# Optimization experiments

Hardware: AMD Instinct MI355X
Metric: run time of the kernel (lower is better)

The kernel has to match this reference:

```python
import jax, jax.numpy as jnp
import numpy as np

# Hough voting constants from the call site:
# Hough(angle=90, R2_list=[4,64,256,1024], num_classes=1, region_num=13, vote_field_size=33)
ANGLE = 90
R2_LIST = (4, 64, 256, 1024)
REGION_NUM = 13
VFS = 33  # vote field size


def _hough_filter():
    """Log-polar vote-field filter [region_num, VFS, VFS].

    Region 0 = center disk (r^2 <= R2_LIST[0]); region 1 + ring*4 + angle_bin
    for the 3 radius rings x 4 angle sectors. Each region's weights are
    1/(#pixels in region) so each region's vote sums to 1 (HoughNet log map).
    """
    c = VFS // 2
    ys, xs = np.meshgrid(np.arange(VFS) - c, np.arange(VFS) - c, indexing='ij')
    r2 = xs ** 2 + ys ** 2
    theta = (np.degrees(np.arctan2(ys, xs)) + 360.0) % 360.0
    nang = 360 // ANGLE  # 4 angle sectors
    abin = np.minimum((theta // ANGLE).astype(np.int64), nang - 1)
    region = -np.ones((VFS, VFS), np.int64)
    region[r2 <= R2_LIST[0]] = 0
    for i in range(1, len(R2_LIST)):
        m = (r2 > R2_LIST[i - 1]) & (r2 <= R2_LIST[i])
        region[m] = 1 + (i - 1) * nang + abin[m]
    filt = np.zeros((REGION_NUM, VFS, VFS), np.float32)
    for r in range(REGION_NUM):
        m = region == r
        if m.sum() > 0:
            filt[r][m] = 1.0 / float(m.sum())
    return filt


# ConvTranspose2d(13 -> 1, k=33, stride=1, pad=16) == SAME conv with flipped kernel.
_HOUGH_CONV_W = jnp.asarray(np.flip(_hough_filter(), axis=(1, 2))[None].copy())  # [1,13,33,33]


def setup_inputs() -> dict:
    key = jax.random.key(0)
    ks = jax.random.split(key, 4)
    B, C, H, W = 2, 256, 256, 512
    return {
        'x': jax.random.normal(ks[0], (B, C, H, W), jnp.float32),
        'pos_w': jax.random.normal(ks[1], (13, C), jnp.float32) * 0.05,
        'pos_b': jnp.zeros((13,), jnp.float32),
        'reg_w': jax.random.normal(ks[2], (1, C), jnp.float32) * 0.05,
        'reg_b': jnp.zeros((1,), jnp.float32),
        'off_w': jax.random.normal(ks[3], (2, C), jnp.float32) * 0.05,
        'off_b': jnp.zeros((2,), jnp.float32),
    }


def _conv1x1(x, w, b):
    # x: [B,C,H,W], w: [O,C] -> [B,O,H,W]
    return jnp.einsum('bchw,oc->bohw', x, w) + b[None, :, None, None]


def reference(x, pos_w, pos_b, reg_w, reg_b, off_w, off_b):
    evident = jax.nn.relu(_conv1x1(x, pos_w, pos_b))  # [B,13,H,W]
    score = jax.lax.conv_general_dilated(
        evident, _HOUGH_CONV_W, (1, 1), 'SAME',
        dimension_numbers=('NCHW', 'OIHW', 'NCHW'))  # [B,1,H,W]
    x_cls = jax.nn.sigmoid(score)
    x_reg = _conv1x1(x, reg_w, reg_b)
    x_off = _conv1x1(x, off_w, off_b)
    return (x_cls, x_reg, x_off)
```

## Files before the change

kernel.cpp:

```cpp
#include <hip/hip_runtime.h>
#include <math.h>

#define BB   2
#define CC   256
#define HH   256
#define WW   512
#define HW   (HH*WW)
#define IMG  (CC*HW)

#define HPP  288
#define WPP  546
#define CHPP (HPP*WPP)
#define EVB2 (13*CHPP)
#define EV2_FLOATS (BB*EVB2)

#define OUT_REG (BB*HW)
#define OUT_OFF (2*BB*HW)

static __device__ __forceinline__ int region_of(int ys, int xs) {
    int r2 = ys * ys + xs * xs;
    int bin;
    if (ys == 0)     bin = (xs >= 0) ? 0 : 2;
    else if (ys > 0) bin = (xs > 0) ? 0 : 1;
    else             bin = (xs < 0) ? 2 : 3;
    if (r2 <= 4)   return 0;
    if (r2 <= 64)  return 1 + bin;
    if (r2 <= 256) return 5 + bin;
    return 9 + bin;
}

__global__ void setup_k(const float* __restrict__ pw, const float* __restrict__ pb,
                        const float* __restrict__ rw, const float* __restrict__ rb,
                        const float* __restrict__ ow, const float* __restrict__ ob,
                        float* __restrict__ wp, float* __restrict__ bias,
                        int2* __restrict__ tabg, int* __restrict__ mg) {
    int blk = blockIdx.x, tid = threadIdx.x;
    if (blk < 16) {
        int i = blk * 256 + tid;
        int c = i >> 4, o = i & 15;
        float v;
        if (o < 13)       v = pw[o * CC + c];
        else if (o == 13) v = rw[c];
        else              v = ow[(o - 14) * CC + c];
        wp[c * 16 + o] = v;
        if (i < 16) {
            float bv = (i < 13) ? pb[i] : (i == 13 ? rb[0] : ob[i - 14]);
            bias[i] = bv;
        }
    } else {
        __shared__ int cnt[13];
        __shared__ int runbuf[33 * 16];
        __shared__ int countrow[33];
        __shared__ int rowstart[34];
        if (tid < 13) cnt[tid] = 0;
        __syncthreads();
        for (int i = tid; i < 1089; i += 256) {
            int ky = i / 33, kx = i - ky * 33;
            atomicAdd(&cnt[region_of(16 - ky, 16 - kx)], 1);
        }
        __syncthreads();
        if (tid < 33) {
            int ky = tid, n = 0;
            int c0 = region_of(16 - ky, 16);
            int kxa = 0;
            for (int kx = 1; kx <= 33; kx++) {
                int c = (kx < 33) ? region_of(16 - ky, 16 - kx) : -1;
                if (c != c0) {
                    runbuf[tid * 16 + n] = c0 | (kxa << 4) | ((kx - 1) << 10);
                    n++;
                    c0 = c; kxa = kx;
                }
            }
            countrow[tid] = n;
        }
        __syncthreads();
        if (tid == 0) {
            int a = 0;
            for (int t = 0; t < 33; t++) { rowstart[t] = a; a += countrow[t]; }
            rowstart[33] = a;
            mg[0] = 2 * a;
        }
        __syncthreads();
        if (tid < 33) {
            int ky = tid, base = rowstart[tid], n = countrow[tid];
            for (int j = 0; j < n; j++) {
                int rn  = runbuf[tid * 16 + j];
                int c   = rn & 15, kxa = (rn >> 4) & 63, kxb = (rn >> 10) & 63;
                float w = 1.0f / (float)cnt[c];
                int off0 = c * CHPP + (ky - 16) * WPP;
                tabg[2 * (base + j)]     = make_int2(off0 + (kxb - 16), __float_as_int(w));
                tabg[2 * (base + j) + 1] = make_int2(off0 + (kxa - 17), __float_as_int(-w));
            }
        }
    }
}

__global__ __launch_bounds__(256) void conv1x1_k(
    const float* __restrict__ x, const float* __restrict__ wp,
    const float* __restrict__ bias, float* __restrict__ ev,
    float* __restrict__ out) {
    int tid = threadIdx.x;
    int g  = blockIdx.x * 256 + tid;
    int p  = g * 2;
    int b  = p >> 17;
    int hw = p & (HW - 1);
    const float* xb = x + (size_t)b * IMG + hw;

    float acc0[16], acc1[16];
#pragma unroll
    for (int o = 0; o < 16; o++) { acc0[o] = 0.f; acc1[o] = 0.f; }

#pragma unroll 4
    for (int c = 0; c < CC; c++) {
        float2 v = *(const float2*)(xb + c * HW);
        const float* wr = wp + c * 16;
#pragma unroll
        for (int o = 0; o < 16; o++) {
            float wv = wr[o];
            acc0[o] = fmaf(v.x, wv, acc0[o]);
            acc1[o] = fmaf(v.y, wv, acc1[o]);
        }
    }

    int y0 = hw >> 9, x0 = hw & 511;
    float* evb = ev + (size_t)b * EVB2 + (y0 + 16) * WPP + (x0 + 18);
#pragma unroll
    for (int o = 0; o < 13; o++) {
        float bo = bias[o];
        *(float2*)(evb + o * CHPP) =
            make_float2(fmaxf(acc0[o] + bo, 0.f), fmaxf(acc1[o] + bo, 0.f));
    }
    float rbv = bias[13];
    *(float2*)(out + OUT_REG + b * HW + hw) = make_float2(acc0[13] + rbv, acc1[13] + rbv);
#pragma unroll
    for (int o = 14; o < 16; o++) {
        float bo = bias[o];
        *(float2*)(out + OUT_OFF + b * 2 * HW + (o - 14) * HW + hw) =
            make_float2(acc0[o] + bo, acc1[o] + bo);
    }
}

__global__ __launch_bounds__(256) void prefix_k(float* __restrict__ ev) {
    int r    = blockIdx.x * 4 + (threadIdx.x >> 6);
    int lane = threadIdx.x & 63;
    if (r >= BB * 13 * HH) return;
    int b   = r / (13 * HH);
    int rem = r - b * (13 * HH);
    int ch  = rem >> 8;
    int y   = rem & 255;
    float* row = ev + (size_t)(b * 13 + ch) * CHPP + (size_t)(y + 16) * WPP;
    float carry = 0.f;
    for (int seg = 0; seg < WPP; seg += 64) {
        int i = seg + lane;
        float v = (i < WPP) ? row[i] : 0.f;
#pragma unroll
        for (int d = 1; d < 64; d <<= 1) {
            float t = __shfl_up(v, d, 64);
            if (lane >= d) v += t;
        }
        v += carry;
        if (i < WPP) row[i] = v;
        carry = __shfl(v, 63, 64);
    }
}

__global__ __launch_bounds__(256) void hough_k(const float* __restrict__ P,
                                               const int2* __restrict__ tabg,
                                               const int* __restrict__ mg,
                                               float* __restrict__ out) {
    int m   = mg[0];
    int tid = threadIdx.x;
    int bid = blockIdx.x;
    int sb  = (bid & 7) * 128 + (bid >> 3);
    int p   = sb * 256 + tid;
    int b   = p >> 17;
    int hw  = p & (HW - 1);
    int y   = hw >> 9, xx = hw & 511;
    const float* Pb = P + (size_t)b * EVB2 + (y + 16) * WPP + (xx + 18);

    float s = 0.f;
#pragma unroll 8
    for (int t = 0; t < m; t++) {
        int2 e = tabg[t];
        s = fmaf(Pb[e.x], __int_as_float(e.y), s);
    }
    out[b * HW + hw] = 1.0f / (1.0f + expf(-s));
}

extern "C" void kernel_launch(void* const* d_in, const int* in_sizes, int n_in,
                              void* d_out, int out_size, void* d_ws, size_t ws_size,
                              hipStream_t stream) {
    const float* x  = (const float*)d_in[0];
    const float* pw = (const float*)d_in[1];
    const float* pb = (const float*)d_in[2];
    const float* rw = (const float*)d_in[3];
    const float* rb = (const float*)d_in[4];
    const float* ow = (const float*)d_in[5];
    const float* ob = (const float*)d_in[6];
    float* out = (float*)d_out;

    float* ev   = (float*)d_ws;
    float* wp   = ev + EV2_FLOATS;
    float* bias = wp + 4096;
    int2*  tabg = (int2*)(bias + 16);
    int*   mg   = (int*)(tabg + 2048);

    hipMemsetAsync(ev, 0, (size_t)EV2_FLOATS * sizeof(float), stream);
    setup_k<<<17, 256, 0, stream>>>(pw, pb, rw, rb, ow, ob, wp, bias, tabg, mg);
    conv1x1_k<<<512, 256, 0, stream>>>(x, wp, bias, ev, out);
    prefix_k<<<1664, 256, 0, stream>>>(ev);
    hough_k<<<1024, 256, 0, stream>>>(ev, tabg, mg, out);
}
```

Baseline: 402.2 us.

## Fuse 1x1 conv with row prefix scan and zero only padding rows

The row-wise prefix scan is folded into the 1x1 conv kernel: each block handles one image row with 512 threads, does wave-level shuffle scans plus a shared-memory cross-wave offset, and writes the scanned evidence directly, including left zero padding and right constant padding. The full-buffer memset is replaced by extra setup blocks that zero only the top and bottom padding rows of each plane. This removes a separate read-modify-write pass over the evidence buffer and a large memset. The cost is one pixel per thread instead of two in the conv, which gives less register-level reuse of the weight loads, and a block-wide barrier.

```diff
diff --git a/kernel.cpp b/kernel.cpp
--- a/kernel.cpp
+++ b/kernel.cpp
@@ -33,7 +33,8 @@
                         const float* __restrict__ rw, const float* __restrict__ rb,
                         const float* __restrict__ ow, const float* __restrict__ ob,
                         float* __restrict__ wp, float* __restrict__ bias,
-                        int2* __restrict__ tabg, int* __restrict__ mg) {
+                        int2* __restrict__ tabg, int* __restrict__ mg,
+                        float* __restrict__ ev) {
     int blk = blockIdx.x, tid = threadIdx.x;
     if (blk < 16) {
         int i = blk * 256 + tid;
@@ -47,7 +48,7 @@
             float bv = (i < 13) ? pb[i] : (i == 13 ? rb[0] : ob[i - 14]);
             bias[i] = bv;
         }
-    } else {
+    } else if (blk == 16) {
         __shared__ int cnt[13];
         __shared__ int runbuf[33 * 16];
         __shared__ int countrow[33];
@@ -92,76 +93,84 @@
                 tabg[2 * (base + j) + 1] = make_int2(off0 + (kxa - 17), __float_as_int(-w));
             }
         }
-    }
-}
-
-__global__ __launch_bounds__(256) void conv1x1_k(
+    } else {
+        int seg   = blk - 17;
+        int plane = seg >> 1;
+        int half  = seg & 1;
+        float* base = ev + (size_t)plane * CHPP + (half ? (size_t)272 * WPP : 0);
+        float4 z = make_float4(0.f, 0.f, 0.f, 0.f);
+        float4* b4 = (float4*)base;
+#pragma unroll
+        for (int it = 0; it < 9; it++) {
+            int idx = it * 256 + tid;
+            if (idx < 2184) b4[idx] = z;
+        }
+    }
+}
+
+__global__ __launch_bounds__(512) void convscan_k(
     const float* __restrict__ x, const float* __restrict__ wp,
     const float* __restrict__ bias, float* __restrict__ ev,
     float* __restrict__ out) {
-    int tid = threadIdx.x;
-    int g  = blockIdx.x * 256 + tid;
-    int p  = g * 2;
-    int b  = p >> 17;
-    int hw = p & (HW - 1);
+    __shared__ float part[13][8];
+    int tid  = threadIdx.x;
+    int lane = tid & 63;
+    int wv   = tid >> 6;
+    int bid  = blockIdx.x;
+    int b    = bid >> 8;
+    int y    = bid & 255;
+    int hw   = y * WW + tid;
     const float* xb = x + (size_t)b * IMG + hw;
 
-    float acc0[16], acc1[16];
-#pragma unroll
-    for (int o = 0; o < 16; o++) { acc0[o] = 0.f; acc1[o] = 0.f; }
+    float acc[16];
+#pragma unroll
+    for (int o = 0; o < 16; o++) acc[o] = 0.f;
 
 #pragma unroll 4
     for (int c = 0; c < CC; c++) {
-        float2 v = *(const float2*)(xb + c * HW);
+        float v = xb[c * HW];
         const float* wr = wp + c * 16;
 #pragma unroll
-        for (int o = 0; o < 16; o++) {
-            float wv = wr[o];
-            acc0[o] = fmaf(v.x, wv, acc0[o]);
-            acc1[o] = fmaf(v.y, wv, acc1[o]);
-        }
-    }
-
-    int y0 = hw >> 9, x0 = hw & 511;
-    float* evb = ev + (size_t)b * EVB2 + (y0 + 16) * WPP + (x0 + 18);
+        for (int o = 0; o < 16; o++) acc[o] = fmaf(v, wr[o], acc[o]);
+    }
+
 #pragma unroll
     for (int o = 0; o < 13; o++) {
-        float bo = bias[o];
-        *(float2*)(evb + o * CHPP) =
-            make_float2(fmaxf(acc0[o] + bo, 0.f), fmaxf(acc1[o] + bo, 0.f));
-    }
-    float rbv = bias[13];
-    *(float2*)(out + OUT_REG + b * HW + hw) = make_float2(acc0[13] + rbv, acc1[13] + rbv);
-#pragma unroll
-    for (int o = 14; o < 16; o++) {
-        float bo = bias[o];
-        *(float2*)(out + OUT_OFF + b * 2 * HW + (o - 14) * HW + hw) =
-            make_float2(acc0[o] + bo, acc1[o] + bo);
-    }
-}
-
-__global__ __launch_bounds__(256) void prefix_k(float* __restrict__ ev) {
-    int r    = blockIdx.x * 4 + (threadIdx.x >> 6);
-    int lane = threadIdx.x & 63;
-    if (r >= BB * 13 * HH) return;
-    int b   = r / (13 * HH);
-    int rem = r - b * (13 * HH);
-    int ch  = rem >> 8;
-    int y   = rem & 255;
-    float* row = ev + (size_t)(b * 13 + ch) * CHPP + (size_t)(y + 16) * WPP;
-    float carry = 0.f;
-    for (int seg = 0; seg < WPP; seg += 64) {
-        int i = seg + lane;
-        float v = (i < WPP) ? row[i] : 0.f;
+        float v = fmaxf(acc[o] + bias[o], 0.f);
 #pragma unroll
         for (int d = 1; d < 64; d <<= 1) {
             float t = __shfl_up(v, d, 64);
             if (lane >= d) v += t;
         }
-        v += carry;
-        if (i < WPP) row[i] = v;
-        carry = __shfl(v, 63, 64);
-    }
+        acc[o] = v;
+        if (lane == 63) part[o][wv] = v;
+    }
+    __syncthreads();
+
+    size_t rowbase = (size_t)(b * 13) * CHPP + (size_t)(y + 16) * WPP;
+#pragma unroll
+    for (int o = 0; o < 13; o++) {
+        float off = 0.f;
+#pragma unroll
+        for (int w2 = 0; w2 < 7; w2++)
+            if (w2 < wv) off += part[o][w2];
+        ev[rowbase + o * CHPP + 18 + tid] = acc[o] + off;
+    }
+    if (tid < 234) {
+        int o = tid / 18, j = tid - o * 18;
+        ev[rowbase + o * CHPP + j] = 0.f;
+    }
+    if (tid < 208) {
+        int o = tid >> 4, j = tid & 15;
+        float tot = 0.f;
+#pragma unroll
+        for (int w2 = 0; w2 < 8; w2++) tot += part[o][w2];
+        ev[rowbase + o * CHPP + 530 + j] = tot;
+    }
+
+    out[OUT_REG + b * HW + hw]          = acc[13] + bias[13];
+    out[OUT_OFF + b * 2 * HW + hw]      = acc[14] + bias[14];
+    out[OUT_OFF + b * 2 * HW + HW + hw] = acc[15] + bias[15];
 }
 
 __global__ __launch_bounds__(256) void hough_k(const float* __restrict__ P,
@@ -205,9 +214,7 @@
     int2*  tabg = (int2*)(bias + 16);
     int*   mg   = (int*)(tabg + 2048);
 
-    hipMemsetAsync(ev, 0, (size_t)EV2_FLOATS * sizeof(float), stream);
-    setup_k<<<17, 256, 0, stream>>>(pw, pb, rw, rb, ow, ob, wp, bias, tabg, mg);
-    conv1x1_k<<<512, 256, 0, stream>>>(x, wp, bias, ev, out);
-    prefix_k<<<1664, 256, 0, stream>>>(ev);
+    setup_k<<<69, 256, 0, stream>>>(pw, pb, rw, rb, ow, ob, wp, bias, tabg, mg, ev);
+    convscan_k<<<512, 512, 0, stream>>>(x, wp, bias, ev, out);
     hough_k<<<1024, 256, 0, stream>>>(ev, tabg, mg, out);
 }
```

After: 397.5 us. About the same (-1.2%).
